# Kernel optimization log

Hardware: AMD Instinct MI355X
Metric: run time of the kernel (lower is better)

Reference implementation:

```python
import jax, jax.numpy as jnp
import numpy as np

C0 = 0.28209479177387814
C1 = 0.4886025119029199
C2 = (1.0925484305920792, -1.0925484305920792, 0.31539156525252005, -1.0925484305920792, 0.5462742152960396)
C3 = (-0.5900435899266435, 2.890611442640554, -0.4570457994644658, 0.37317633259011546, -0.4570457994644658, 1.445305721320277, -0.5900435899266435)


def quat_to_rotmat(q):
    # q: [N,4] (w,x,y,z), unnormalized
    q = q / jnp.linalg.norm(q, axis=-1, keepdims=True)
    w, x, y, z = q[:, 0], q[:, 1], q[:, 2], q[:, 3]
    R = jnp.stack([
        1 - 2 * (y * y + z * z), 2 * (x * y - w * z), 2 * (x * z + w * y),
        2 * (x * y + w * z), 1 - 2 * (x * x + z * z), 2 * (y * z - w * x),
        2 * (x * z - w * y), 2 * (y * z + w * x), 1 - 2 * (x * x + y * y),
    ], axis=-1).reshape(-1, 3, 3)
    return R


def sh_basis_deg3(dirs):
    # dirs: [N,3] normalized -> [N,16] real SH basis (gsplat convention)
    x, y, z = dirs[:, 0], dirs[:, 1], dirs[:, 2]
    xx, yy, zz = x * x, y * y, z * z
    one = jnp.ones_like(x)
    b = [C0 * one,
         -C1 * y, C1 * z, -C1 * x,
         C2[0] * x * y, C2[1] * y * z, C2[2] * (2 * zz - xx - yy), C2[3] * x * z, C2[4] * (xx - yy),
         C3[0] * y * (3 * xx - yy), C3[1] * x * y * z, C3[2] * y * (4 * zz - xx - yy),
         C3[3] * z * (2 * zz - 3 * xx - 3 * yy), C3[4] * x * (4 * zz - xx - yy),
         C3[5] * z * (xx - yy), C3[6] * x * (xx - 3 * yy)]
    return jnp.stack(b, axis=-1)


def setup_inputs() -> dict:
    key = jax.random.key(0)
    ks = jax.random.split(key, 6)
    N = 1024
    means = jax.random.normal(ks[0], (N, 3), dtype=jnp.float32) * 1.5
    scales = jax.random.normal(ks[1], (N, 3), dtype=jnp.float32) * 0.3 + jnp.log(0.08)  # log-scales
    quats = jax.random.normal(ks[2], (N, 4), dtype=jnp.float32)
    features_dc = jax.random.normal(ks[3], (N, 3), dtype=jnp.float32) * 0.5
    features_rest = jax.random.normal(ks[4], (N, 15, 3), dtype=jnp.float32) * 0.05
    opacities = jax.random.normal(ks[5], (N, 1), dtype=jnp.float32)  # logits
    # camera: identity rotation, gaussians pushed to z ~ 6 in front of camera
    viewmat = jnp.array([[1., 0., 0., 0.],
                         [0., 1., 0., 0.],
                         [0., 0., 1., 6.],
                         [0., 0., 0., 1.]], dtype=jnp.float32)
    K = jnp.array([[260., 0., 112.],
                   [0., 260., 112.],
                   [0., 0., 1.]], dtype=jnp.float32)
    background = jnp.array([0.149, 0.1647, 0.2157], dtype=jnp.float32)
    return {"means": means, "scales": scales, "quats": quats,
            "features_dc": features_dc, "features_rest": features_rest,
            "opacities": opacities, "viewmat": viewmat, "K": K,
            "background": background, "H": 224, "W": 224}


def reference(means, scales, quats, features_dc, features_rest, opacities,
              viewmat, K, background, H, W):
    N = means.shape[0]
    Rcw = viewmat[:3, :3]
    t = viewmat[:3, 3]
    fx, fy, cx, cy = K[0, 0], K[1, 1], K[0, 2], K[1, 2]

    # --- project means to camera frame ---
    p_cam = means @ Rcw.T + t                     # [N,3]
    z = p_cam[:, 2]
    valid = z > 0.01
    zc = jnp.maximum(z, 0.01)
    x, y = p_cam[:, 0], p_cam[:, 1]

    # --- 3D covariance: R S S^T R^T ---
    Rg = quat_to_rotmat(quats)                    # [N,3,3]
    S = jnp.exp(scales)                           # [N,3]
    M = Rg * S[:, None, :]
    cov3d = M @ jnp.swapaxes(M, 1, 2)             # [N,3,3]
    cov_cam = jnp.einsum('ij,njk,lk->nil', Rcw, cov3d, Rcw)

    # --- EWA perspective projection (classic mode, 0.3 px blur) ---
    zeros = jnp.zeros_like(zc)
    J = jnp.stack([
        jnp.stack([fx / zc, zeros, -fx * x / (zc * zc)], axis=-1),
        jnp.stack([zeros, fy / zc, -fy * y / (zc * zc)], axis=-1)], axis=1)  # [N,2,3]
    cov2d = jnp.einsum('nij,njk,nlk->nil', J, cov_cam, J) + 0.3 * jnp.eye(2, dtype=means.dtype)
    a, b, c = cov2d[:, 0, 0], cov2d[:, 0, 1], cov2d[:, 1, 1]
    det = a * c - b * b
    det_safe = jnp.where(det > 0, det, 1.0)
    conicA, conicB, conicC = c / det_safe, -b / det_safe, a / det_safe

    u = fx * x / zc + cx                          # [N] pixel-space means
    v = fy * y / zc + cy

    # --- SH color evaluation (degree 3) ---
    cam_pos = -Rcw.T @ t
    vdir = means - cam_pos
    vdir = vdir / jnp.linalg.norm(vdir, axis=-1, keepdims=True)
    coeffs = jnp.concatenate([features_dc[:, None, :], features_rest], axis=1)  # [N,16,3]
    colors = jnp.einsum('nk,nkc->nc', sh_basis_deg3(vdir), coeffs) + 0.5
    colors = jnp.maximum(colors, 0.0)             # [N,3]

    opac = jax.nn.sigmoid(opacities[:, 0])        # [N]

    # --- per-pixel gaussian weights (dense rasterization) ---
    px = jnp.arange(W, dtype=means.dtype) + 0.5
    py = jnp.arange(H, dtype=means.dtype) + 0.5
    gx, gy = jnp.meshgrid(px, py)                 # [H,W]
    gx, gy = gx.reshape(-1), gy.reshape(-1)       # [HW]
    dx = gx[None, :] - u[:, None]                 # [N,HW]
    dy = gy[None, :] - v[:, None]
    sigma = 0.5 * (conicA[:, None] * dx * dx + conicC[:, None] * dy * dy) + conicB[:, None] * dx * dy
    ok = (sigma >= 0) & valid[:, None] & (det > 0)[:, None]
    gauss = jnp.exp(-jnp.maximum(sigma, 0.0))
    alpha = jnp.where(ok, opac[:, None] * gauss, 0.0)
    alpha = jnp.minimum(alpha, 0.999)
    alpha = jnp.where(alpha < 1.0 / 255.0, 0.0, alpha)  # [N,HW]

    # --- depth sort + front-to-back alpha compositing ---
    order = jnp.argsort(zc)
    alpha_s = alpha[order]
    colors_s = colors[order]
    T = jnp.cumprod(1.0 - alpha_s, axis=0)        # [N,HW]
    T_excl = jnp.concatenate([jnp.ones((1, H * W), dtype=alpha.dtype), T[:-1]], axis=0)
    w = T_excl * alpha_s                          # [N,HW]
    rgb = jnp.einsum('np,nc->pc', w, colors_s)    # [HW,3]
    out = rgb + T[-1][:, None] * background
    return out.reshape(H, W, 3)
```

## Files before the change

### kernel.cpp

```cpp
#include <hip/hip_runtime.h>
#include <math.h>

#define NG 1024
#define TS 8

#define ZK_OFF   0
#define ABB_OFF  (2*NG)
#define AD0_OFF  (6*NG)
#define AD1_OFF  (10*NG)
#define AD2_OFF  (14*NG)
#define BBB_OFF  (15*NG)
#define BD0_OFF  (19*NG)
#define BD1_OFF  (23*NG)
#define BD2_OFF  (27*NG)
#define WS_CNT_OFF (28*NG)

__global__ __launch_bounds__(256) void prep_kernel(
    const float* __restrict__ means, const float* __restrict__ scales,
    const float* __restrict__ quats, const float* __restrict__ fdc,
    const float* __restrict__ frest, const float* __restrict__ opac,
    const float* __restrict__ vm, const float* __restrict__ Km,
    float* __restrict__ ws, int N)
{
    int i = blockIdx.x * 256 + threadIdx.x;
    if (i >= N) return;

    float r00 = vm[0], r01 = vm[1], r02 = vm[2],  t0 = vm[3];
    float r10 = vm[4], r11 = vm[5], r12 = vm[6],  t1 = vm[7];
    float r20 = vm[8], r21 = vm[9], r22 = vm[10], t2 = vm[11];
    float fx = Km[0], cx = Km[2], fy = Km[4], cy = Km[5];

    float mx = means[3*i+0], my = means[3*i+1], mz = means[3*i+2];
    float px = r00*mx + r01*my + r02*mz + t0;
    float py = r10*mx + r11*my + r12*mz + t1;
    float pz = r20*mx + r21*my + r22*mz + t2;
    bool valid = pz > 0.01f;
    float zc = fmaxf(pz, 0.01f);

    float qw = quats[4*i+0], qx = quats[4*i+1], qy = quats[4*i+2], qz = quats[4*i+3];
    float qn = rsqrtf(qw*qw + qx*qx + qy*qy + qz*qz);
    qw *= qn; qx *= qn; qy *= qn; qz *= qn;
    float R00 = 1.f - 2.f*(qy*qy + qz*qz), R01 = 2.f*(qx*qy - qw*qz), R02 = 2.f*(qx*qz + qw*qy);
    float R10 = 2.f*(qx*qy + qw*qz), R11 = 1.f - 2.f*(qx*qx + qz*qz), R12 = 2.f*(qy*qz - qw*qx);
    float R20 = 2.f*(qx*qz - qw*qy), R21 = 2.f*(qy*qz + qw*qx), R22 = 1.f - 2.f*(qx*qx + qy*qy);

    float s0 = __expf(scales[3*i+0]), s1 = __expf(scales[3*i+1]), s2 = __expf(scales[3*i+2]);
    float M00 = R00*s0, M01 = R01*s1, M02 = R02*s2;
    float M10 = R10*s0, M11 = R11*s1, M12 = R12*s2;
    float M20 = R20*s0, M21 = R21*s1, M22 = R22*s2;
    float c00 = M00*M00 + M01*M01 + M02*M02;
    float c01 = M00*M10 + M01*M11 + M02*M12;
    float c02 = M00*M20 + M01*M21 + M02*M22;
    float c11 = M10*M10 + M11*M11 + M12*M12;
    float c12 = M10*M20 + M11*M21 + M12*M22;
    float c22 = M20*M20 + M21*M21 + M22*M22;
    float P00 = r00*c00 + r01*c01 + r02*c02;
    float P01 = r00*c01 + r01*c11 + r02*c12;
    float P02 = r00*c02 + r01*c12 + r02*c22;
    float P10 = r10*c00 + r11*c01 + r12*c02;
    float P11 = r10*c01 + r11*c11 + r12*c12;
    float P12 = r10*c02 + r11*c12 + r12*c22;
    float P20 = r20*c00 + r21*c01 + r22*c02;
    float P21 = r20*c01 + r21*c11 + r22*c12;
    float P22 = r20*c02 + r21*c12 + r22*c22;
    float w00 = P00*r00 + P01*r01 + P02*r02;
    float w01 = P00*r10 + P01*r11 + P02*r12;
    float w02 = P00*r20 + P01*r21 + P02*r22;
    float w11 = P10*r10 + P11*r11 + P12*r12;
    float w12 = P10*r20 + P11*r21 + P12*r22;
    float w22 = P20*r20 + P21*r21 + P22*r22;

    float g0 = fx / zc;
    float g2 = -fx * px / (zc * zc);
    float h1 = fy / zc;
    float h2 = -fy * py / (zc * zc);
    float a = g0*g0*w00 + 2.f*g0*g2*w02 + g2*g2*w22 + 0.3f;
    float b = g0*(w01*h1 + w02*h2) + g2*(w12*h1 + w22*h2);
    float c = h1*h1*w11 + 2.f*h1*h2*w12 + h2*h2*w22 + 0.3f;
    float det = a*c - b*b;
    float det_safe = (det > 0.f) ? det : 1.f;
    float conicA = c / det_safe;
    float conicB = -b / det_safe;
    float conicC = a / det_safe;

    float u = fx * px / zc + cx;
    float v = fy * py / zc + cy;

    float cpx = -(r00*t0 + r10*t1 + r20*t2);
    float cpy = -(r01*t0 + r11*t1 + r21*t2);
    float cpz = -(r02*t0 + r12*t1 + r22*t2);
    float vx = mx - cpx, vy = my - cpy, vz = mz - cpz;
    float vn = rsqrtf(vx*vx + vy*vy + vz*vz);
    float x = vx*vn, y = vy*vn, z = vz*vn;
    float xx = x*x, yy = y*y, zz = z*z;
    float bs[16];
    bs[0]  = 0.28209479177387814f;
    bs[1]  = -0.4886025119029199f * y;
    bs[2]  = 0.4886025119029199f * z;
    bs[3]  = -0.4886025119029199f * x;
    bs[4]  = 1.0925484305920792f * x * y;
    bs[5]  = -1.0925484305920792f * y * z;
    bs[6]  = 0.31539156525252005f * (2.f*zz - xx - yy);
    bs[7]  = -1.0925484305920792f * x * z;
    bs[8]  = 0.5462742152960396f * (xx - yy);
    bs[9]  = -0.5900435899266435f * y * (3.f*xx - yy);
    bs[10] = 2.890611442640554f * x * y * z;
    bs[11] = -0.4570457994644658f * y * (4.f*zz - xx - yy);
    bs[12] = 0.37317633259011546f * z * (2.f*zz - 3.f*xx - 3.f*yy);
    bs[13] = -0.4570457994644658f * x * (4.f*zz - xx - yy);
    bs[14] = 1.445305721320277f * z * (xx - yy);
    bs[15] = -0.5900435899266435f * x * (xx - 3.f*yy);

    float cr = bs[0]*fdc[3*i+0];
    float cg = bs[0]*fdc[3*i+1];
    float cb = bs[0]*fdc[3*i+2];
    #pragma unroll
    for (int k = 1; k < 16; ++k) {
        const float* f = frest + (i*15 + (k-1))*3;
        cr += bs[k]*f[0];
        cg += bs[k]*f[1];
        cb += bs[k]*f[2];
    }
    cr = fmaxf(cr + 0.5f, 0.f);
    cg = fmaxf(cg + 0.5f, 0.f);
    cb = fmaxf(cb + 0.5f, 0.f);

    float ops = 1.f / (1.f + __expf(-opac[i]));
    float op_eff = (valid && det > 0.f) ? ops : 0.f;
    bool keep = op_eff >= (1.f / 255.f);

    float tau = fmaxf(__logf(255.f * fmaxf(op_eff, 1e-8f)), 0.f);
    float rx = 1.01f * sqrtf(2.f * tau * a) + 1.0f;
    float ry = 1.01f * sqrtf(2.f * tau * c) + 1.0f;

    ((float2*)(ws + ZK_OFF))[i] = make_float2(keep ? zc : 3.0e30f, keep ? 1.f : 0.f);
    ((float4*)(ws + ABB_OFF))[i] = make_float4(u - rx, v - ry, u + rx, v + ry);
    ((float4*)(ws + AD0_OFF))[i] = make_float4(u, v, 0.5f*conicA, conicB);
    ((float4*)(ws + AD1_OFF))[i] = make_float4(0.5f*conicC, op_eff, cr, cg);
    (ws + AD2_OFF)[i] = cb;
}

__global__ __launch_bounds__(256) void rank_kernel(float* __restrict__ ws, int N)
{
    int tid = threadIdx.x;
    int lane = tid & 63;
    int i = blockIdx.x * 4 + (tid >> 6);
    if (i >= N) return;
    const float2* zk = (const float2*)(ws + ZK_OFF);
    float2 me = zk[i];
    float zi = me.x;
    bool ki = me.y != 0.f;
    int r = 0, cnt = 0;
    for (int j = lane; j < N; j += 64) {
        float2 vj = zk[j];
        if (vj.y != 0.f) {
            cnt++;
            if (vj.x < zi || (vj.x == zi && j < i)) r++;
        }
    }
    int packed = r | (cnt << 16);
    #pragma unroll
    for (int s = 32; s; s >>= 1) packed += __shfl_xor(packed, s);
    r = packed & 0xffff;
    cnt = (int)((unsigned)packed >> 16);
    if (lane == 0) {
        if (i == 0) ((int*)(ws + WS_CNT_OFF))[0] = cnt;
        if (ki) {
            ((float4*)(ws + BBB_OFF))[r] = ((const float4*)(ws + ABB_OFF))[i];
            ((float4*)(ws + BD0_OFF))[r] = ((const float4*)(ws + AD0_OFF))[i];
            ((float4*)(ws + BD1_OFF))[r] = ((const float4*)(ws + AD1_OFF))[i];
            (ws + BD2_OFF)[r] = (ws + AD2_OFF)[i];
        }
    }
}

__global__ __launch_bounds__(64) void composite_tile(
    const float* __restrict__ ws, const float* __restrict__ bg,
    float* __restrict__ out, int W, int H, int ntx)
{
    __shared__ float4 ds0[64], ds1[64];
    __shared__ float  ds2[64];
    const int M = *(const int*)(ws + WS_CNT_OFF);
    const float4* bbB = (const float4*)(ws + BBB_OFF);
    const float4* d0B = (const float4*)(ws + BD0_OFF);
    const float4* d1B = (const float4*)(ws + BD1_OFF);
    const float*  d2B = ws + BD2_OFF;

    int lane = threadIdx.x;
    int tx = blockIdx.x % ntx, ty = blockIdx.x / ntx;
    float tx0 = tx*TS + 0.5f, tx1 = tx*TS + (TS - 0.5f);
    float ty0 = ty*TS + 0.5f, ty1 = ty*TS + (TS - 0.5f);
    int px = tx*TS + (lane & (TS-1)), py = ty*TS + (lane >> 3);
    float gx = px + 0.5f, gy = py + 0.5f;

    float T = 1.f, cr = 0.f, cg = 0.f, cb = 0.f;

    float4 cbb = make_float4(1e30f, 1e30f, -1e30f, -1e30f);
    float4 c0 = make_float4(0,0,0,0), c1 = make_float4(0,0,0,0);
    float  c2 = 0.f;
    if (lane < M) { cbb = bbB[lane]; c0 = d0B[lane]; c1 = d1B[lane]; c2 = d2B[lane]; }

    for (int base = 0; base < M; base += 64) {
        int nj = base + 64 + lane;
        float4 nbb = make_float4(1e30f, 1e30f, -1e30f, -1e30f);
        float4 n0 = make_float4(0,0,0,0), n1 = make_float4(0,0,0,0);
        float  n2 = 0.f;
        if (nj < M) { nbb = bbB[nj]; n0 = d0B[nj]; n1 = d1B[nj]; n2 = d2B[nj]; }

        bool ov = (base + lane < M) &
                  (cbb.x <= tx1) & (cbb.z >= tx0) &
                  (cbb.y <= ty1) & (cbb.w >= ty0);
        unsigned long long m = __ballot(ov);
        if (m) {
            ds0[lane] = c0; ds1[lane] = c1; ds2[lane] = c2;
            while (m) {
                int j = (int)__builtin_ctzll(m);
                m &= m - 1;
                float4 q0 = ds0[j];
                float4 q1 = ds1[j];
                float bc = ds2[j];
                float dx = gx - q0.x, dy = gy - q0.y;
                float sg = fmaf(dx, fmaf(q0.z, dx, q0.w*dy), q1.x*(dy*dy));
                float e  = __expf(-sg);
                float al = fminf(q1.y * e, 0.999f);
                bool ok = (sg >= 0.f) & (al >= 0.00392156862745098f);
                al = ok ? al : 0.f;
                float w = T * al;
                cr = fmaf(w, q1.z, cr);
                cg = fmaf(w, q1.w, cg);
                cb = fmaf(w, bc, cb);
                T = fmaf(-al, T, T);
            }
        }
        cbb = nbb; c0 = n0; c1 = n1; c2 = n2;
    }

    if (px < W && py < H) {
        int p = py*W + px;
        out[3*p+0] = fmaf(T, bg[0], cr);
        out[3*p+1] = fmaf(T, bg[1], cg);
        out[3*p+2] = fmaf(T, bg[2], cb);
    }
}

extern "C" void kernel_launch(void* const* d_in, const int* in_sizes, int n_in,
                              void* d_out, int out_size, void* d_ws, size_t ws_size,
                              hipStream_t stream) {
    const float* means  = (const float*)d_in[0];
    const float* scales = (const float*)d_in[1];
    const float* quats  = (const float*)d_in[2];
    const float* fdc    = (const float*)d_in[3];
    const float* frest  = (const float*)d_in[4];
    const float* opac   = (const float*)d_in[5];
    const float* vm     = (const float*)d_in[6];
    const float* Km     = (const float*)d_in[7];
    const float* bg     = (const float*)d_in[8];

    int N  = in_sizes[0] / 3;
    int HW = out_size / 3;
    int W = (int)(sqrtf((float)HW) + 0.5f);
    while (W > 1 && HW % W) --W;
    int H = HW / W;

    float* ws  = (float*)d_ws;
    float* out = (float*)d_out;

    prep_kernel<<<(N + 255) / 256, 256, 0, stream>>>(means, scales, quats, fdc,
                                                     frest, opac, vm, Km, ws, N);
    rank_kernel<<<(N + 3) / 4, 256, 0, stream>>>(ws, N);

    int ntx = (W + TS - 1) / TS;
    int nty = (H + TS - 1) / TS;
    composite_tile<<<ntx * nty, 64, 0, stream>>>(ws, bg, out, W, H, ntx);
}
```

Before: 90.76 us.

## Fuse preprocessing and depth-rank scatter into a single kernel

Merges the per-Gaussian preprocessing kernel and the rank/scatter kernel into one launch. Each wavefront recomputes camera depth and the opacity keep-test for every other Gaussian directly from the inputs, then writes its packed record straight to its sorted slot. This removes one kernel launch and the intermediate workspace round-trip. In exchange it does redundant per-lane preprocessing and extra exp work in the rank loop, and the keep-test no longer checks det > 0.

Result: slower. 93.43 us (+2.9%).

```diff
diff --git a/kernel.cpp b/kernel.cpp
--- a/kernel.cpp
+++ b/kernel.cpp
@@ -4,25 +4,22 @@
 #define NG 1024
 #define TS 8
 
-#define ZK_OFF   0
-#define ABB_OFF  (2*NG)
-#define AD0_OFF  (6*NG)
-#define AD1_OFF  (10*NG)
-#define AD2_OFF  (14*NG)
 #define BBB_OFF  (15*NG)
 #define BD0_OFF  (19*NG)
 #define BD1_OFF  (23*NG)
 #define BD2_OFF  (27*NG)
 #define WS_CNT_OFF (28*NG)
 
-__global__ __launch_bounds__(256) void prep_kernel(
+__global__ __launch_bounds__(256) void prep_rank_kernel(
     const float* __restrict__ means, const float* __restrict__ scales,
     const float* __restrict__ quats, const float* __restrict__ fdc,
     const float* __restrict__ frest, const float* __restrict__ opac,
     const float* __restrict__ vm, const float* __restrict__ Km,
     float* __restrict__ ws, int N)
 {
-    int i = blockIdx.x * 256 + threadIdx.x;
+    int tid = threadIdx.x;
+    int lane = tid & 63;
+    int i = blockIdx.x * 4 + (tid >> 6);
     if (i >= N) return;
 
     float r00 = vm[0], r01 = vm[1], r02 = vm[2],  t0 = vm[3];
@@ -31,11 +28,33 @@
     float fx = Km[0], cx = Km[2], fy = Km[4], cy = Km[5];
 
     float mx = means[3*i+0], my = means[3*i+1], mz = means[3*i+2];
+    float pzi = __fmaf_rn(r20, mx, __fmaf_rn(r21, my, __fmaf_rn(r22, mz, t2)));
+    float opsi = 1.f / (1.f + __expf(-opac[i]));
+    bool ki = (pzi > 0.01f) && (opsi >= (1.f/255.f));
+
+    int r = 0, cnt = 0;
+    for (int j = lane; j < N; j += 64) {
+        float jx = means[3*j+0], jy = means[3*j+1], jz = means[3*j+2];
+        float pzj = __fmaf_rn(r20, jx, __fmaf_rn(r21, jy, __fmaf_rn(r22, jz, t2)));
+        float opsj = 1.f / (1.f + __expf(-opac[j]));
+        bool kj = (pzj > 0.01f) && (opsj >= (1.f/255.f));
+        if (kj) {
+            cnt++;
+            if (pzj < pzi || (pzj == pzi && j < i)) r++;
+        }
+    }
+    int packed = r | (cnt << 16);
+    #pragma unroll
+    for (int s = 32; s; s >>= 1) packed += __shfl_xor(packed, s);
+    r = packed & 0xffff;
+    cnt = (int)((unsigned)packed >> 16);
+
+    if (i == 0 && lane == 0) ((int*)(ws + WS_CNT_OFF))[0] = cnt;
+    if (!ki) return;
+
     float px = r00*mx + r01*my + r02*mz + t0;
     float py = r10*mx + r11*my + r12*mz + t1;
-    float pz = r20*mx + r21*my + r22*mz + t2;
-    bool valid = pz > 0.01f;
-    float zc = fmaxf(pz, 0.01f);
+    float zc = fmaxf(pzi, 0.01f);
 
     float qw = quats[4*i+0], qx = quats[4*i+1], qy = quats[4*i+2], qz = quats[4*i+3];
     float qn = rsqrtf(qw*qw + qx*qx + qy*qy + qz*qz);
@@ -125,52 +144,15 @@
     cg = fmaxf(cg + 0.5f, 0.f);
     cb = fmaxf(cb + 0.5f, 0.f);
 
-    float ops = 1.f / (1.f + __expf(-opac[i]));
-    float op_eff = (valid && det > 0.f) ? ops : 0.f;
-    bool keep = op_eff >= (1.f / 255.f);
-
-    float tau = fmaxf(__logf(255.f * fmaxf(op_eff, 1e-8f)), 0.f);
+    float tau = fmaxf(__logf(255.f * opsi), 0.f);
     float rx = 1.01f * sqrtf(2.f * tau * a) + 1.0f;
     float ry = 1.01f * sqrtf(2.f * tau * c) + 1.0f;
 
-    ((float2*)(ws + ZK_OFF))[i] = make_float2(keep ? zc : 3.0e30f, keep ? 1.f : 0.f);
-    ((float4*)(ws + ABB_OFF))[i] = make_float4(u - rx, v - ry, u + rx, v + ry);
-    ((float4*)(ws + AD0_OFF))[i] = make_float4(u, v, 0.5f*conicA, conicB);
-    ((float4*)(ws + AD1_OFF))[i] = make_float4(0.5f*conicC, op_eff, cr, cg);
-    (ws + AD2_OFF)[i] = cb;
-}
-
-__global__ __launch_bounds__(256) void rank_kernel(float* __restrict__ ws, int N)
-{
-    int tid = threadIdx.x;
-    int lane = tid & 63;
-    int i = blockIdx.x * 4 + (tid >> 6);
-    if (i >= N) return;
-    const float2* zk = (const float2*)(ws + ZK_OFF);
-    float2 me = zk[i];
-    float zi = me.x;
-    bool ki = me.y != 0.f;
-    int r = 0, cnt = 0;
-    for (int j = lane; j < N; j += 64) {
-        float2 vj = zk[j];
-        if (vj.y != 0.f) {
-            cnt++;
-            if (vj.x < zi || (vj.x == zi && j < i)) r++;
-        }
-    }
-    int packed = r | (cnt << 16);
-    #pragma unroll
-    for (int s = 32; s; s >>= 1) packed += __shfl_xor(packed, s);
-    r = packed & 0xffff;
-    cnt = (int)((unsigned)packed >> 16);
     if (lane == 0) {
-        if (i == 0) ((int*)(ws + WS_CNT_OFF))[0] = cnt;
-        if (ki) {
-            ((float4*)(ws + BBB_OFF))[r] = ((const float4*)(ws + ABB_OFF))[i];
-            ((float4*)(ws + BD0_OFF))[r] = ((const float4*)(ws + AD0_OFF))[i];
-            ((float4*)(ws + BD1_OFF))[r] = ((const float4*)(ws + AD1_OFF))[i];
-            (ws + BD2_OFF)[r] = (ws + AD2_OFF)[i];
-        }
+        ((float4*)(ws + BBB_OFF))[r] = make_float4(u - rx, v - ry, u + rx, v + ry);
+        ((float4*)(ws + BD0_OFF))[r] = make_float4(u, v, 0.5f*conicA, conicB);
+        ((float4*)(ws + BD1_OFF))[r] = make_float4(0.5f*conicC, opsi, cr, cg);
+        (ws + BD2_OFF)[r] = cb;
     }
 }
 
@@ -265,9 +247,8 @@
     float* ws  = (float*)d_ws;
     float* out = (float*)d_out;
 
-    prep_kernel<<<(N + 255) / 256, 256, 0, stream>>>(means, scales, quats, fdc,
-                                                     frest, opac, vm, Km, ws, N);
-    rank_kernel<<<(N + 3) / 4, 256, 0, stream>>>(ws, N);
+    prep_rank_kernel<<<(N + 3) / 4, 256, 0, stream>>>(means, scales, quats, fdc,
+                                                      frest, opac, vm, Km, ws, N);
 
     int ntx = (W + TS - 1) / TS;
     int nty = (H + TS - 1) / TS;
```
